# Performance work log

Measured on AMD Instinct MI355X. Metric: run time of the kernel, lower is better.

## Reference

```python
import jax, jax.numpy as jnp
import numpy as np

N, K, C, D4, HID, HEAD, DEPTH = 40000, 16, 128, 32, 512, 256, 4
EPS = 1e-5  # BatchNorm eps; eval mode with running_mean=0, running_var=1


def _bn(x, g, b):
    # eval-mode BatchNorm1d with fresh running stats (mean=0, var=1)
    return x * (g / np.sqrt(1.0 + EPS)) + b


def _mlp(x, w1, b1, w2, g, b):
    # Linear -> GELU -> Linear(no bias) -> BN
    return _bn(jax.nn.gelu(x @ w1 + b1) @ w2, g, b)


def _lfp(x, lxyz, knn, proj, coor, scale, g, b):
    # LFP: Linear(no bias) -> la_spse_a4 (neighbor gather + anisotropic spatial
    # positional encoding, one PE channel per 4 feature channels, max-pool over k) -> BN
    xp = x @ proj                                   # (N, C)
    xn = xp[knn]                                    # (N, K, C) irregular gather
    rel3 = (lxyz[knn] - lxyz[:, None])[..., :3]     # (N, K, 3)
    pe = jnp.einsum('nkc,cd->nkd', rel3, coor) * jnp.square(scale)  # (N, K, D4)
    out = jnp.max(xn.reshape(N, K, D4, 4) + pe[..., None], axis=1).reshape(N, C)
    return _bn(out, g, b)


def _knn_spse4(lxyz, feat, knn, m_sp, c, h):
    # knn_spse_4: squared anisotropic spatial distances (3 learned 4-d directions
    # per output channel, 12 params) + per-channel color (3) + height (1) weighted
    # squared diffs, averaged over k neighbors; caller takes sqrt.
    rel4 = lxyz[knn] - lxyz[:, None]                # (N, K, 4)
    relf = feat[knn] - feat[:, None]                # (N, K, 4) = color(3)+height(1)
    dirs = m_sp.reshape(3, 4, C)
    e = jnp.zeros((N, K, C), jnp.float32)
    for j in range(3):  # fixed small loop over 3 learned directions
        e = e + jnp.square(jnp.einsum('nkc,cd->nkd', rel4, dirs[j]))
    e = e + jnp.einsum('nki,id->nkd', jnp.square(relf[..., :3]), jnp.square(c))
    e = e + jnp.square(relf[..., 3:4]) * jnp.square(h)
    return jnp.sqrt(e.mean(axis=1))                 # (N, C)


def setup_inputs():
    key = jax.random.key(0)
    ks = jax.random.split(key, 32)
    rn = lambda i, s, sc=0.02: jax.random.normal(ks[i], s, jnp.float32) * sc
    gm = lambda i, s: 1.0 + jax.random.normal(ks[i], s, jnp.float32) * 0.1
    return {
        'x': rn(0, (N, 4), 1.0),
        'xyz': jax.random.uniform(ks[1], (N, 3), jnp.float32),
        'knn': jax.random.randint(ks[2], (N, K), 0, N, jnp.int32),
        'spse_m': rn(3, (12, C), 0.5),
        'spse_c': rn(4, (3, C), 0.5),
        'spse_h': rn(5, (C,), 0.5),
        'nbr_bn0_g': gm(6, (C,)), 'nbr_bn0_b': rn(7, (C,)),
        'nbr_w1': rn(8, (C, 2 * C)), 'nbr_b1': rn(9, (2 * C,)),
        'nbr_w2': rn(10, (2 * C, C)),
        'nbr_bn_g': gm(11, (C,)), 'nbr_bn_b': rn(12, (C,)),
        'lfp_proj': rn(13, (DEPTH, C, C)),
        'lfp_coor': rn(14, (DEPTH, 3, D4), 0.5),
        'lfp_scale': 0.1 + rn(15, (DEPTH, D4), 0.01),
        'lfp_bng': gm(16, (DEPTH, C)), 'lfp_bnb': rn(17, (DEPTH, C)),
        'mlp_w1': rn(18, (3, C, HID)), 'mlp_b1': rn(19, (3, HID)),
        'mlp_w2': rn(20, (3, HID, C)),
        'mlp_bng': gm(21, (3, C)), 'mlp_bnb': rn(22, (3, C)),
        'post_bn_g': gm(23, (C,)), 'post_bn_b': rn(24, (C,)),
        'post_w': rn(25, (C, HEAD)),
    }


def reference(x, xyz, knn, spse_m, spse_c, spse_h, nbr_bn0_g, nbr_bn0_b,
              nbr_w1, nbr_b1, nbr_w2, nbr_bn_g, nbr_bn_b,
              lfp_proj, lfp_coor, lfp_scale, lfp_bng, lfp_bnb,
              mlp_w1, mlp_b1, mlp_w2, mlp_bng, mlp_bnb,
              post_bn_g, post_bn_b, post_w):
    # Stage.forward, first==last stage, eval mode (no drop_path, no closs).
    lxyz = jnp.pad(xyz, ((0, 0), (0, 1)))  # cor_std = 1.0
    nbr = _knn_spse4(lxyz, x, knn, spse_m, spse_c, spse_h)
    nbr = _bn(nbr, nbr_bn0_g, nbr_bn0_b)
    nbr = jax.nn.gelu(nbr @ nbr_w1 + nbr_b1) @ nbr_w2   # nbr_proj
    h = _bn(nbr, nbr_bn_g, nbr_bn_b)                    # nbr_bn; x = nbr (first stage)
    # Block: residual MLP, then DEPTH LFPs with an MLP after every 2nd LFP
    h = h + _mlp(h, mlp_w1[0], mlp_b1[0], mlp_w2[0], mlp_bng[0], mlp_bnb[0])
    for i in range(DEPTH):
        h = h + _lfp(h, lxyz, knn, lfp_proj[i], lfp_coor[i], lfp_scale[i],
                     lfp_bng[i], lfp_bnb[i])
        if i % 2 == 1:
            j = i // 2 + 1
            h = h + _mlp(h, mlp_w1[j], mlp_b1[j], mlp_w2[j], mlp_bng[j], mlp_bnb[j])
    return _bn(h, post_bn_g, post_bn_b) @ post_w        # postproj -> (N, HEAD)
```

## Files before the change

kernel.cpp:

```cpp
#include <hip/hip_runtime.h>
#include <hip/hip_bf16.h>
#include <math.h>

#define NPTS 40000
#define KNB 16
#define CH 128

typedef unsigned short u16;
typedef __attribute__((ext_vector_type(8))) short bf16x8;
typedef __attribute__((ext_vector_type(4))) float f32x4;

__device__ __forceinline__ float gelu_f(float v) {
  const float u = 0.7978845608028654f * (v + 0.044715f * v * v * v);
  const float t = __builtin_amdgcn_exp2f(-2.8853900817779268f * u);
  return v * __builtin_amdgcn_rcpf(1.0f + t);
}

__device__ __forceinline__ float bnscale(float g) {
  return g * rsqrtf(1.0f + 1e-5f);
}

__device__ __forceinline__ u16 f2bf(float x) {
  union { __hip_bfloat16 b; u16 u; } cv;
  cv.b = __float2bfloat16(x);
  return cv.u;
}

__device__ __forceinline__ float bf2f(u16 u) {
  union { float f; unsigned int i; } cv;
  cv.i = ((unsigned int)u) << 16;
  return cv.f;
}

__device__ __forceinline__ void bf16split(float x, u16& hi, u16& lo) {
  hi = f2bf(x);
  lo = f2bf(x - bf2f(hi));
}

__device__ __forceinline__ void gl2lds(const u16* gp, u16* lp) {
  __builtin_amdgcn_global_load_lds(
      (const __attribute__((address_space(1))) void*)gp,
      (__attribute__((address_space(3))) void*)lp, 16, 0, 0);
}

__global__ __launch_bounds__(128) void spse_kernel(
    const float* __restrict__ x, const float* __restrict__ xyz,
    const int* __restrict__ knn, const float* __restrict__ sm,
    const float* __restrict__ sc, const float* __restrict__ sh,
    const float* __restrict__ g0, const float* __restrict__ b0,
    u16* __restrict__ oh, u16* __restrict__ ol) {
  const int n = blockIdx.x;
  const int c = threadIdx.x;
  __shared__ float sr[KNB][3];
  __shared__ float sf[KNB][4];
  if (c < KNB) {
    const int j = knn[n * KNB + c];
    sr[c][0] = xyz[j * 3 + 0] - xyz[n * 3 + 0];
    sr[c][1] = xyz[j * 3 + 1] - xyz[n * 3 + 1];
    sr[c][2] = xyz[j * 3 + 2] - xyz[n * 3 + 2];
    float f0 = x[j * 4 + 0] - x[n * 4 + 0];
    float f1 = x[j * 4 + 1] - x[n * 4 + 1];
    float f2 = x[j * 4 + 2] - x[n * 4 + 2];
    float f3 = x[j * 4 + 3] - x[n * 4 + 3];
    sf[c][0] = f0 * f0; sf[c][1] = f1 * f1;
    sf[c][2] = f2 * f2; sf[c][3] = f3 * f3;
  }
  __syncthreads();
  const float m0 = sm[c], m1 = sm[CH + c], m2 = sm[2 * CH + c];
  const float m4 = sm[4 * CH + c], m5 = sm[5 * CH + c], m6 = sm[6 * CH + c];
  const float m8 = sm[8 * CH + c], m9 = sm[9 * CH + c], m10 = sm[10 * CH + c];
  float c0 = sc[c];          c0 *= c0;
  float c1 = sc[CH + c];     c1 *= c1;
  float c2 = sc[2 * CH + c]; c2 *= c2;
  float h2 = sh[c];          h2 *= h2;
  float e = 0.0f;
#pragma unroll
  for (int k = 0; k < KNB; k++) {
    const float r0 = sr[k][0], r1 = sr[k][1], r2 = sr[k][2];
    const float d0 = fmaf(r2, m2, fmaf(r1, m1, r0 * m0));
    const float d1 = fmaf(r2, m6, fmaf(r1, m5, r0 * m4));
    const float d2 = fmaf(r2, m10, fmaf(r1, m9, r0 * m8));
    e = fmaf(d0, d0, e);
    e = fmaf(d1, d1, e);
    e = fmaf(d2, d2, e);
    e = fmaf(sf[k][0], c0, e);
    e = fmaf(sf[k][1], c1, e);
    e = fmaf(sf[k][2], c2, e);
    e = fmaf(sf[k][3], h2, e);
  }
  const float v = sqrtf(e * (1.0f / KNB)) * bnscale(g0[c]) + b0[c];
  u16 hi, lo; bf16split(v, hi, lo);
  const size_t idx = (size_t)n * CH + c;
  oh[idx] = hi; ol[idx] = lo;
}

template <bool XP>
__global__ __launch_bounds__(256, 4) void lfp_kernel(
    const u16* __restrict__ xp, const int* __restrict__ knn,
    const float* __restrict__ xyz, const float* __restrict__ coor,
    const float* __restrict__ scale, const float* __restrict__ g,
    const float* __restrict__ b, const u16* __restrict__ pjh,
    const u16* __restrict__ pjl, u16* __restrict__ xpo,
    u16* __restrict__ hh, u16* __restrict__ hl) {
  const int t = threadIdx.x;
  const int bid = blockIdx.x;
  __shared__ int si[16][KNB];
  __shared__ float sr[16][KNB][3];
  __shared__ __align__(16) u16 Hs[16 * 128];
  {
    const int pp = t >> 4, kk = t & 15;
    const int n = bid * 16 + pp;
    const int j = knn[n * KNB + kk];
    si[pp][kk] = j;
    sr[pp][kk][0] = xyz[j * 3 + 0] - xyz[n * 3 + 0];
    sr[pp][kk][1] = xyz[j * 3 + 1] - xyz[n * 3 + 1];
    sr[pp][kk][2] = xyz[j * 3 + 2] - xyz[n * 3 + 2];
  }
  __syncthreads();
  const int p = t >> 4, d8 = t & 15;
  const int n = bid * 16 + p;

  bf16x8 v[KNB];
#pragma unroll
  for (int k = 0; k < KNB; k++)
    v[k] = *(const bf16x8*)(xp + (size_t)si[p][k] * CH + d8 * 8);

  const float c0a = coor[d8 * 2],     c1a = coor[32 + d8 * 2],     c2a = coor[64 + d8 * 2];
  const float c0b = coor[d8 * 2 + 1], c1b = coor[32 + d8 * 2 + 1], c2b = coor[64 + d8 * 2 + 1];
  float s2a = scale[d8 * 2];     s2a *= s2a;
  float s2b = scale[d8 * 2 + 1]; s2b *= s2b;
  float a[8];
#pragma unroll
  for (int e = 0; e < 8; e++) a[e] = -3.0e38f;
#pragma unroll
  for (int k = 0; k < KNB; k++) {
    const float r0 = sr[p][k][0], r1 = sr[p][k][1], r2 = sr[p][k][2];
    const float pea = fmaf(r2, c2a, fmaf(r1, c1a, r0 * c0a)) * s2a;
    const float peb = fmaf(r2, c2b, fmaf(r1, c1b, r0 * c0b)) * s2b;
#pragma unroll
    for (int e = 0; e < 4; e++) a[e] = fmaxf(a[e], bf2f((u16)v[k][e]) + pea);
#pragma unroll
    for (int e = 4; e < 8; e++) a[e] = fmaxf(a[e], bf2f((u16)v[k][e]) + peb);
  }
  const size_t off = (size_t)n * CH + d8 * 8;
  union { u16 a[8]; uint4 v; } ih, il, oh, ol;
  ih.v = *(const uint4*)(hh + off);
  il.v = *(const uint4*)(hl + off);
#pragma unroll
  for (int e = 0; e < 8; e++) {
    const int c = d8 * 8 + e;
    const float nv = bf2f(ih.a[e]) + bf2f(il.a[e]) + a[e] * bnscale(g[c]) + b[c];
    u16 hi, lo; bf16split(nv, hi, lo);
    oh.a[e] = hi; ol.a[e] = lo;
  }
  *(uint4*)(hh + off) = oh.v;
  *(uint4*)(hl + off) = ol.v;

  if constexpr (XP) {
    {
      const int c0 = d8 * 8;
      const int cs0 = (c0 & ~63) | ((c0 & 63) ^ ((p & 7) << 3));
      *(uint4*)(Hs + p * 128 + cs0) = oh.v;
    }
    __syncthreads();
    const int lane = t & 63, w = t >> 6;
    const int lc = lane & 15, lq = lane >> 4;
    const int lq8 = lq * 8, lq4 = lq * 4;
    bf16x8 ph_[2][4], pl_[2][4];
#pragma unroll
    for (int nf = 0; nf < 2; nf++)
#pragma unroll
      for (int ks = 0; ks < 4; ks++) {
        const size_t wo = (size_t)(w * 32 + nf * 16 + lc) * 128 + ks * 32 + lq8;
        ph_[nf][ks] = *(const bf16x8*)(pjh + wo);
        pl_[nf][ks] = *(const bf16x8*)(pjl + wo);
      }
    const f32x4 zz = {0.0f, 0.0f, 0.0f, 0.0f};
    f32x4 xacc[2] = {zz, zz};
#pragma unroll
    for (int ks = 0; ks < 4; ks++) {
      const int j = ks * 32 + lq8;
      const int cs = (j & ~63) | ((j & 63) ^ ((lc & 7) << 3));
      const bf16x8 aF = *(const bf16x8*)(Hs + lc * 128 + cs);
#pragma unroll
      for (int nf = 0; nf < 2; nf++) {
        xacc[nf] = __builtin_amdgcn_mfma_f32_16x16x32_bf16(aF, ph_[nf][ks], xacc[nf], 0, 0, 0);
        xacc[nf] = __builtin_amdgcn_mfma_f32_16x16x32_bf16(aF, pl_[nf][ks], xacc[nf], 0, 0, 0);
      }
    }
#pragma unroll
    for (int q = 0; q < 4; q++)
#pragma unroll
      for (int nf = 0; nf < 2; nf++)
        xpo[(size_t)(bid * 16 + lq4 + q) * CH + w * 32 + nf * 16 + lc] =
            f2bf(xacc[nf][q]);
  }
}

__global__ __launch_bounds__(256) void prep_weights(
    const float* __restrict__ nw1, const float* __restrict__ nw2,
    const float* __restrict__ mw1, const float* __restrict__ mw2,
    const float* __restrict__ lproj, const float* __restrict__ pw,
    const float* __restrict__ pg, u16* __restrict__ th, u16* __restrict__ tl) {
  const int idx = blockIdx.x * 256 + threadIdx.x;
  const float* src;
  int local, Kd, Nd, dst, swz;
  float scale = 1.0f;
  if (idx < 32768)        { src = nw1; local = idx;          Kd = 128; Nd = 256; dst = 0; swz = 0; }
  else if (idx < 65536)   { src = nw2; local = idx - 32768;  Kd = 256; Nd = 128; dst = 32768; swz = 1; }
  else if (idx < 262144)  { int j = (idx - 65536) >> 16;  local = (idx - 65536) & 65535;
                            src = mw1 + j * 65536; Kd = 128; Nd = 512; dst = 65536 + j * 65536; swz = 0; }
  else if (idx < 458752)  { int j = (idx - 262144) >> 16; local = (idx - 262144) & 65535;
                            src = mw2 + j * 65536; Kd = 512; Nd = 128; dst = 262144 + j * 65536; swz = 1; }
  else if (idx < 524288)  { int i = (idx - 458752) >> 14; local = (idx - 458752) & 16383;
                            src = lproj + i * 16384; Kd = 128; Nd = 128; dst = 458752 + i * 16384; swz = 0; }
  else if (idx < 557056)  { local = idx - 524288; src = pw; Kd = 128; Nd = 256; dst = 524288; swz = 0;
                            scale = bnscale(pg[local >> 8]); }
  else return;
  const int k = local / Nd, n = local % Nd;
  const float v = src[local] * scale;
  u16 hi, lo; bf16split(v, hi, lo);
  const int ks = swz ? ((k & ~63) | ((k & 63) ^ ((n & 7) << 3))) : k;
  const int o = dst + n * Kd + ks;
  th[o] = hi; tl[o] = lo;
}

__global__ __launch_bounds__(256) void fold_pb(const float* __restrict__ pw,
                                               const float* __restrict__ pb,
                                               float* __restrict__ fb) {
  const int t = threadIdx.x;
  float a = 0.0f;
  for (int k = 0; k < 128; k++) a = fmaf(pb[k], pw[k * 256 + t], a);
  fb[t] = a;
}

template <int EPI, int NSPLIT>
__global__ __launch_bounds__(256, 2) void k128_reg(
    const u16* __restrict__ Ahi, const u16* __restrict__ Alo,
    const u16* __restrict__ Wth, const u16* __restrict__ Wtl,
    const float* __restrict__ p0, u16* __restrict__ outu,
    float* __restrict__ outf, int ostride, int ntiles) {
  const int t = threadIdx.x, lane = t & 63, w = t >> 6;
  const int col0 = blockIdx.y * 128;
  const int wm0 = (w >> 1) * 32, wn0 = (w & 1) * 64;
  const int lc = lane & 15, lq = lane >> 4;
  const int lq8 = lq * 8, lq4 = lq * 4;

  bf16x8 wh[4][4], wl[4][4];
  float bv[4];
#pragma unroll
  for (int nf = 0; nf < 4; nf++) {
    const int nr = col0 + wn0 + nf * 16 + lc;
    const u16* wr = Wth + (size_t)nr * 128;
    const u16* wr2 = Wtl + (size_t)nr * 128;
#pragma unroll
    for (int ks = 0; ks < 4; ks++) {
      wh[nf][ks] = *(const bf16x8*)(wr + ks * 32 + lq8);
      wl[nf][ks] = *(const bf16x8*)(wr2 + ks * 32 + lq8);
    }
    bv[nf] = p0[nr];
  }

  const f32x4 zz = {0.0f, 0.0f, 0.0f, 0.0f};
  for (int tile = blockIdx.x; tile < ntiles; tile += gridDim.x) {
    const int row0 = tile * 64;
    f32x4 acc[2][4];
#pragma unroll
    for (int mf = 0; mf < 2; mf++)
#pragma unroll
      for (int nf = 0; nf < 4; nf++) acc[mf][nf] = zz;
#pragma unroll
    for (int ks = 0; ks < 4; ks++) {
      bf16x8 ah[2], al[2];
#pragma unroll
      for (int mf = 0; mf < 2; mf++) {
        const size_t ao = (size_t)(row0 + wm0 + mf * 16 + lc) * 128 + ks * 32 + lq8;
        ah[mf] = *(const bf16x8*)(Ahi + ao);
        if (NSPLIT == 3) al[mf] = *(const bf16x8*)(Alo + ao);
      }
#pragma unroll
      for (int mf = 0; mf < 2; mf++)
#pragma unroll
        for (int nf = 0; nf < 4; nf++) {
          acc[mf][nf] = __builtin_amdgcn_mfma_f32_16x16x32_bf16(ah[mf], wh[nf][ks], acc[mf][nf], 0, 0, 0);
          acc[mf][nf] = __builtin_amdgcn_mfma_f32_16x16x32_bf16(ah[mf], wl[nf][ks], acc[mf][nf], 0, 0, 0);
          if (NSPLIT == 3)
            acc[mf][nf] = __builtin_amdgcn_mfma_f32_16x16x32_bf16(al[mf], wh[nf][ks], acc[mf][nf], 0, 0, 0);
        }
    }
#pragma unroll
    for (int mf = 0; mf < 2; mf++)
#pragma unroll
      for (int q = 0; q < 4; q++) {
        const int r = row0 + wm0 + mf * 16 + lq4 + q;
#pragma unroll
        for (int nf = 0; nf < 4; nf++) {
          const int col = col0 + wn0 + nf * 16 + lc;
          const size_t off = (size_t)r * ostride + col;
          const float v = acc[mf][nf][q];
          if (EPI == 1) outu[off] = f2bf(gelu_f(v + bv[nf]));
          else          outf[off] = v + bv[nf];
        }
      }
  }
}

template <int K, bool RES, bool XP>
__global__ __launch_bounds__(256, 3) void gemm_w2(
    const u16* __restrict__ A, const u16* __restrict__ Wth,
    const u16* __restrict__ Wtl, const float* __restrict__ g,
    const float* __restrict__ bb, const u16* __restrict__ pjh,
    const u16* __restrict__ pjl, u16* __restrict__ xpo,
    u16* __restrict__ hh, u16* __restrict__ hl) {
  __shared__ __align__(16) u16 Ws[2][128 * 64];
  const int t = threadIdx.x, lane = t & 63, w = t >> 6;
  const int row0 = blockIdx.x * 64;
  const int wm0 = (w >> 1) * 32, wn0 = (w & 1) * 64;
  const int lc = lane & 15, lq = lane >> 4;
  const int lq8 = lq * 8, lq4 = lq * 4;

  const f32x4 zz = {0.0f, 0.0f, 0.0f, 0.0f};
  f32x4 acc[2][4];
#pragma unroll
  for (int mf = 0; mf < 2; mf++)
#pragma unroll
    for (int nf = 0; nf < 4; nf++) acc[mf][nf] = zz;

  auto stage_slab = [&](u16* lds, int kb) {
#pragma unroll
    for (int i = 0; i < 1024; i += 256) {
      const int wc0 = i + w * 64;
      const int c = wc0 + lane;
      gl2lds(Wth + (size_t)(c >> 3) * K + kb + (c & 7) * 8, lds + wc0 * 8);
    }
  };
  auto load_af = [&](bf16x8 (&dst)[2][2], int kb) {
#pragma unroll
    for (int mf = 0; mf < 2; mf++)
#pragma unroll
      for (int ks = 0; ks < 2; ks++)
        dst[mf][ks] = *(const bf16x8*)(A + (size_t)(row0 + wm0 + mf * 16 + lc) * K +
                                       kb + ks * 32 + lq8);
  };

  bf16x8 afc[2][2], afn[2][2];
  stage_slab(Ws[0], 0);
  load_af(afc, 0);
  __syncthreads();

  constexpr int NT = K / 64;
#pragma unroll 2
  for (int tt = 0; tt < NT; tt++) {
    const int cur = tt & 1;
    if (tt + 1 < NT) {
      stage_slab(Ws[cur ^ 1], (tt + 1) * 64);
      load_af(afn, (tt + 1) * 64);
    }
#pragma unroll
    for (int ks = 0; ks < 2; ks++) {
      bf16x8 whf[4], wlf[4];
#pragma unroll
      for (int nf = 0; nf < 4; nf++) {
        const int nr = wn0 + nf * 16 + lc;
        const int j = (ks * 32 + lq8) ^ ((nr & 7) << 3);
        whf[nf] = *(const bf16x8*)(Ws[cur] + nr * 64 + j);
        wlf[nf] = *(const bf16x8*)(Wtl + (size_t)nr * K + tt * 64 + j);
      }
#pragma unroll
      for (int mf = 0; mf < 2; mf++)
#pragma unroll
        for (int nf = 0; nf < 4; nf++) {
          acc[mf][nf] = __builtin_amdgcn_mfma_f32_16x16x32_bf16(afc[mf][ks], whf[nf], acc[mf][nf], 0, 0, 0);
          acc[mf][nf] = __builtin_amdgcn_mfma_f32_16x16x32_bf16(afc[mf][ks], wlf[nf], acc[mf][nf], 0, 0, 0);
        }
    }
    __syncthreads();
#pragma unroll
    for (int mf = 0; mf < 2; mf++)
#pragma unroll
      for (int ks = 0; ks < 2; ks++) afc[mf][ks] = afn[mf][ks];
  }

  u16* Hs = &Ws[0][0];
  float S0[4], S1[4];
#pragma unroll
  for (int nf = 0; nf < 4; nf++) {
    const int col = wn0 + nf * 16 + lc;
    S0[nf] = bnscale(g[col]);
    S1[nf] = bb[col];
  }
#pragma unroll
  for (int mf = 0; mf < 2; mf++)
#pragma unroll
    for (int q = 0; q < 4; q++) {
      const int r = row0 + wm0 + mf * 16 + lq4 + q;
#pragma unroll
      for (int nf = 0; nf < 4; nf++) {
        const int col = wn0 + nf * 16 + lc;
        const size_t off = (size_t)r * CH + col;
        float v = acc[mf][nf][q] * S0[nf] + S1[nf];
        if (RES) v += bf2f(hh[off]) + bf2f(hl[off]);
        u16 hi, lo; bf16split(v, hi, lo);
        hh[off] = hi; hl[off] = lo;
        if constexpr (XP) {
          const int rl = wm0 + mf * 16 + lq4 + q;
          const int cs = (col & ~63) | ((col & 63) ^ ((rl & 7) << 3));
          Hs[rl * 128 + cs] = hi;
        }
      }
    }

  if constexpr (XP) {
    __syncthreads();
    bf16x8 ph_[2][4], pl_[2][4];
#pragma unroll
    for (int nf = 0; nf < 2; nf++)
#pragma unroll
      for (int ks = 0; ks < 4; ks++) {
        const size_t wo = (size_t)(w * 32 + nf * 16 + lc) * 128 + ks * 32 + lq8;
        ph_[nf][ks] = *(const bf16x8*)(pjh + wo);
        pl_[nf][ks] = *(const bf16x8*)(pjl + wo);
      }
    f32x4 xacc[4][2];
#pragma unroll
    for (int mf = 0; mf < 4; mf++)
#pragma unroll
      for (int nf = 0; nf < 2; nf++) xacc[mf][nf] = zz;
#pragma unroll
    for (int ks = 0; ks < 4; ks++) {
      const int j = ks * 32 + lq8;
      bf16x8 aF[4];
#pragma unroll
      for (int mf = 0; mf < 4; mf++) {
        const int r = mf * 16 + lc;
        const int cs = (j & ~63) | ((j & 63) ^ ((r & 7) << 3));
        aF[mf] = *(const bf16x8*)(Hs + r * 128 + cs);
      }
#pragma unroll
      for (int mf = 0; mf < 4; mf++)
#pragma unroll
        for (int nf = 0; nf < 2; nf++) {
          xacc[mf][nf] = __builtin_amdgcn_mfma_f32_16x16x32_bf16(aF[mf], ph_[nf][ks], xacc[mf][nf], 0, 0, 0);
          xacc[mf][nf] = __builtin_amdgcn_mfma_f32_16x16x32_bf16(aF[mf], pl_[nf][ks], xacc[mf][nf], 0, 0, 0);
        }
    }
#pragma unroll
    for (int mf = 0; mf < 4; mf++)
#pragma unroll
      for (int q = 0; q < 4; q++)
#pragma unroll
        for (int nf = 0; nf < 2; nf++)
          xpo[(size_t)(row0 + mf * 16 + lq4 + q) * CH + w * 32 + nf * 16 + lc] =
              f2bf(xacc[mf][nf][q]);
  }
}

extern "C" void kernel_launch(void* const* d_in, const int* in_sizes, int n_in,
                              void* d_out, int out_size, void* d_ws, size_t ws_size,
                              hipStream_t stream) {
  const float* x    = (const float*)d_in[0];
  const float* xyz  = (const float*)d_in[1];
  const int*   knn  = (const int*)d_in[2];
  const float* sm   = (const float*)d_in[3];
  const float* scc  = (const float*)d_in[4];
  const float* shh  = (const float*)d_in[5];
  const float* bn0g = (const float*)d_in[6];
  const float* bn0b = (const float*)d_in[7];
  const float* nw1  = (const float*)d_in[8];
  const float* nb1  = (const float*)d_in[9];
  const float* nw2  = (const float*)d_in[10];
  const float* nbng = (const float*)d_in[11];
  const float* nbnb = (const float*)d_in[12];
  const float* lproj  = (const float*)d_in[13];
  const float* lcoor  = (const float*)d_in[14];
  const float* lscale = (const float*)d_in[15];
  const float* lbng   = (const float*)d_in[16];
  const float* lbnb   = (const float*)d_in[17];
  const float* mw1  = (const float*)d_in[18];
  const float* mb1  = (const float*)d_in[19];
  const float* mw2  = (const float*)d_in[20];
  const float* mbng = (const float*)d_in[21];
  const float* mbnb = (const float*)d_in[22];
  const float* pg   = (const float*)d_in[23];
  const float* pb   = (const float*)d_in[24];
  const float* pw   = (const float*)d_in[25];
  float* out = (float*)d_out;

  char* ws = (char*)d_ws;
  u16*   h_hi = (u16*)(ws + 0);
  u16*   h_lo = (u16*)(ws + 10240000);
  u16*   act  = (u16*)(ws + 20480000);
  u16*   xpA  = (u16*)(ws + 61440000);
  u16*   xpB  = (u16*)(ws + 71680000);
  u16*   Wh   = (u16*)(ws + 81920000);
  u16*   Wl   = (u16*)(ws + 83034112);
  float* fb   = (float*)(ws + 84148224);

  const u16* nw1t   = Wh + 0;
  const u16* nw2t   = Wh + 32768;
  const u16* mw1t   = Wh + 65536;
  const u16* mw2t   = Wh + 262144;
  const u16* lprojt = Wh + 458752;
  const u16* postt  = Wh + 524288;
  const u16* nw1tl   = Wl + 0;
  const u16* nw2tl   = Wl + 32768;
  const u16* mw1tl   = Wl + 65536;
  const u16* mw2tl   = Wl + 262144;
  const u16* lprojtl = Wl + 458752;
  const u16* posttl  = Wl + 524288;

  prep_weights<<<2176, 256, 0, stream>>>(nw1, nw2, mw1, mw2, lproj, pw, pg, Wh, Wl);
  fold_pb<<<1, 256, 0, stream>>>(pw, pb, fb);

  spse_kernel<<<NPTS, 128, 0, stream>>>(x, xyz, knn, sm, scc, shh, bn0g, bn0b, h_hi, h_lo);

  k128_reg<1, 2><<<dim3(256, 2), 256, 0, stream>>>(h_hi, h_lo, nw1t, nw1tl, nb1,
                                                   act, nullptr, 256, 625);
  gemm_w2<256, false, false><<<625, 256, 0, stream>>>(
      act, nw2t, nw2tl, nbng, nbnb, nullptr, nullptr, nullptr, h_hi, h_lo);

  k128_reg<1, 2><<<dim3(128, 4), 256, 0, stream>>>(h_hi, h_lo, mw1t, mw1tl, mb1,
                                                   act, nullptr, 512, 625);
  gemm_w2<512, true, true><<<625, 256, 0, stream>>>(
      act, mw2t, mw2tl, mbng, mbnb, lprojt, lprojtl, xpA, h_hi, h_lo);

  lfp_kernel<true><<<2500, 256, 0, stream>>>(
      xpA, knn, xyz, lcoor + 0 * 96, lscale + 0 * 32, lbng + 0 * 128, lbnb + 0 * 128,
      lprojt + 16384, lprojtl + 16384, xpB, h_hi, h_lo);

  lfp_kernel<false><<<2500, 256, 0, stream>>>(
      xpB, knn, xyz, lcoor + 1 * 96, lscale + 1 * 32, lbng + 1 * 128, lbnb + 1 * 128,
      nullptr, nullptr, nullptr, h_hi, h_lo);
  k128_reg<1, 2><<<dim3(128, 4), 256, 0, stream>>>(h_hi, h_lo, mw1t + 65536,
                                                   mw1tl + 65536, mb1 + 512,
                                                   act, nullptr, 512, 625);
  gemm_w2<512, true, true><<<625, 256, 0, stream>>>(
      act, mw2t + 65536, mw2tl + 65536, mbng + 128, mbnb + 128,
      lprojt + 2 * 16384, lprojtl + 2 * 16384, xpA, h_hi, h_lo);

  lfp_kernel<true><<<2500, 256, 0, stream>>>(
      xpA, knn, xyz, lcoor + 2 * 96, lscale + 2 * 32, lbng + 2 * 128, lbnb + 2 * 128,
      lprojt + 3 * 16384, lprojtl + 3 * 16384, xpB, h_hi, h_lo);

  lfp_kernel<false><<<2500, 256, 0, stream>>>(
      xpB, knn, xyz, lcoor + 3 * 96, lscale + 3 * 32, lbng + 3 * 128, lbnb + 3 * 128,
      nullptr, nullptr, nullptr, h_hi, h_lo);
  k128_reg<1, 2><<<dim3(128, 4), 256, 0, stream>>>(h_hi, h_lo, mw1t + 2 * 65536,
                                                   mw1tl + 2 * 65536, mb1 + 2 * 512,
                                                   act, nullptr, 512, 625);
  gemm_w2<512, true, false><<<625, 256, 0, stream>>>(
      act, mw2t + 2 * 65536, mw2tl + 2 * 65536, mbng + 2 * 128, mbnb + 2 * 128,
      nullptr, nullptr, nullptr, h_hi, h_lo);

  k128_reg<2, 3><<<dim3(256, 2), 256, 0, stream>>>(h_hi, h_lo, postt, posttl, fb,
                                                   nullptr, out, 256, 625);
}
```

Before: 428.4 us.

## Store LFP projections channel-blocked and split LFP gather by channel quarter

The xp projection buffer changes from point-major [N][128] to four channel-quarter blocks [4][N][32], so each LFP block gathers neighbours from a 2.56 MB slice that fits in cache better. The LFP kernel now handles 64 points times one 32-channel quarter per block. It also issues the residual loads early behind a sched_barrier. The projection previously fused into the LFP kernel moves into a separate k128_reg GEMM launch with a new EPI==0 path that writes the blocked layout. This adds two kernel launches and an extra round trip of h through memory, in exchange for better gather locality.

```diff
diff --git a/kernel.cpp b/kernel.cpp
--- a/kernel.cpp
+++ b/kernel.cpp
@@ -94,22 +94,20 @@
   oh[idx] = hi; ol[idx] = lo;
 }
 
-template <bool XP>
 __global__ __launch_bounds__(256, 4) void lfp_kernel(
     const u16* __restrict__ xp, const int* __restrict__ knn,
     const float* __restrict__ xyz, const float* __restrict__ coor,
     const float* __restrict__ scale, const float* __restrict__ g,
-    const float* __restrict__ b, const u16* __restrict__ pjh,
-    const u16* __restrict__ pjl, u16* __restrict__ xpo,
-    u16* __restrict__ hh, u16* __restrict__ hl) {
+    const float* __restrict__ b, u16* __restrict__ hh, u16* __restrict__ hl) {
   const int t = threadIdx.x;
   const int bid = blockIdx.x;
-  __shared__ int si[16][KNB];
-  __shared__ float sr[16][KNB][3];
-  __shared__ __align__(16) u16 Hs[16 * 128];
-  {
-    const int pp = t >> 4, kk = t & 15;
-    const int n = bid * 16 + pp;
+  const int q = bid & 3;
+  const int pg = bid >> 2;
+  __shared__ int si[64][KNB];
+  __shared__ float sr[64][KNB][3];
+  for (int i = t; i < 64 * KNB; i += 256) {
+    const int pp = i >> 4, kk = i & 15;
+    const int n = pg * 64 + pp;
     const int j = knn[n * KNB + kk];
     si[pp][kk] = j;
     sr[pp][kk][0] = xyz[j * 3 + 0] - xyz[n * 3 + 0];
@@ -117,18 +115,27 @@
     sr[pp][kk][2] = xyz[j * 3 + 2] - xyz[n * 3 + 2];
   }
   __syncthreads();
-  const int p = t >> 4, d8 = t & 15;
-  const int n = bid * 16 + p;
-
+  const int p = t >> 2;
+  const int l = t & 3;
+  const int n = pg * 64 + p;
+  const int cbase = q * 32 + l * 8;
+  const int d0 = cbase >> 2;
+
+  const u16* xpq = xp + (size_t)q * NPTS * 32;
   bf16x8 v[KNB];
 #pragma unroll
   for (int k = 0; k < KNB; k++)
-    v[k] = *(const bf16x8*)(xp + (size_t)si[p][k] * CH + d8 * 8);
-
-  const float c0a = coor[d8 * 2],     c1a = coor[32 + d8 * 2],     c2a = coor[64 + d8 * 2];
-  const float c0b = coor[d8 * 2 + 1], c1b = coor[32 + d8 * 2 + 1], c2b = coor[64 + d8 * 2 + 1];
-  float s2a = scale[d8 * 2];     s2a *= s2a;
-  float s2b = scale[d8 * 2 + 1]; s2b *= s2b;
+    v[k] = *(const bf16x8*)(xpq + (size_t)si[p][k] * 32 + l * 8);
+  const size_t off = (size_t)n * CH + cbase;
+  union { u16 a[8]; uint4 v; } ih, il, oh, ol;
+  ih.v = *(const uint4*)(hh + off);
+  il.v = *(const uint4*)(hl + off);
+  __builtin_amdgcn_sched_barrier(0);
+
+  const float c0a = coor[d0],     c1a = coor[32 + d0],     c2a = coor[64 + d0];
+  const float c0b = coor[d0 + 1], c1b = coor[32 + d0 + 1], c2b = coor[64 + d0 + 1];
+  float s2a = scale[d0];     s2a *= s2a;
+  float s2b = scale[d0 + 1]; s2b *= s2b;
   float a[8];
 #pragma unroll
   for (int e = 0; e < 8; e++) a[e] = -3.0e38f;
@@ -142,59 +149,15 @@
 #pragma unroll
     for (int e = 4; e < 8; e++) a[e] = fmaxf(a[e], bf2f((u16)v[k][e]) + peb);
   }
-  const size_t off = (size_t)n * CH + d8 * 8;
-  union { u16 a[8]; uint4 v; } ih, il, oh, ol;
-  ih.v = *(const uint4*)(hh + off);
-  il.v = *(const uint4*)(hl + off);
 #pragma unroll
   for (int e = 0; e < 8; e++) {
-    const int c = d8 * 8 + e;
+    const int c = cbase + e;
     const float nv = bf2f(ih.a[e]) + bf2f(il.a[e]) + a[e] * bnscale(g[c]) + b[c];
     u16 hi, lo; bf16split(nv, hi, lo);
     oh.a[e] = hi; ol.a[e] = lo;
   }
   *(uint4*)(hh + off) = oh.v;
   *(uint4*)(hl + off) = ol.v;
-
-  if constexpr (XP) {
-    {
-      const int c0 = d8 * 8;
-      const int cs0 = (c0 & ~63) | ((c0 & 63) ^ ((p & 7) << 3));
-      *(uint4*)(Hs + p * 128 + cs0) = oh.v;
-    }
-    __syncthreads();
-    const int lane = t & 63, w = t >> 6;
-    const int lc = lane & 15, lq = lane >> 4;
-    const int lq8 = lq * 8, lq4 = lq * 4;
-    bf16x8 ph_[2][4], pl_[2][4];
-#pragma unroll
-    for (int nf = 0; nf < 2; nf++)
-#pragma unroll
-      for (int ks = 0; ks < 4; ks++) {
-        const size_t wo = (size_t)(w * 32 + nf * 16 + lc) * 128 + ks * 32 + lq8;
-        ph_[nf][ks] = *(const bf16x8*)(pjh + wo);
-        pl_[nf][ks] = *(const bf16x8*)(pjl + wo);
-      }
-    const f32x4 zz = {0.0f, 0.0f, 0.0f, 0.0f};
-    f32x4 xacc[2] = {zz, zz};
-#pragma unroll
-    for (int ks = 0; ks < 4; ks++) {
-      const int j = ks * 32 + lq8;
-      const int cs = (j & ~63) | ((j & 63) ^ ((lc & 7) << 3));
-      const bf16x8 aF = *(const bf16x8*)(Hs + lc * 128 + cs);
-#pragma unroll
-      for (int nf = 0; nf < 2; nf++) {
-        xacc[nf] = __builtin_amdgcn_mfma_f32_16x16x32_bf16(aF, ph_[nf][ks], xacc[nf], 0, 0, 0);
-        xacc[nf] = __builtin_amdgcn_mfma_f32_16x16x32_bf16(aF, pl_[nf][ks], xacc[nf], 0, 0, 0);
-      }
-    }
-#pragma unroll
-    for (int q = 0; q < 4; q++)
-#pragma unroll
-      for (int nf = 0; nf < 2; nf++)
-        xpo[(size_t)(bid * 16 + lq4 + q) * CH + w * 32 + nf * 16 + lc] =
-            f2bf(xacc[nf][q]);
-  }
 }
 
 __global__ __launch_bounds__(256) void prep_weights(
@@ -258,7 +221,7 @@
       wh[nf][ks] = *(const bf16x8*)(wr + ks * 32 + lq8);
       wl[nf][ks] = *(const bf16x8*)(wr2 + ks * 32 + lq8);
     }
-    bv[nf] = p0[nr];
+    bv[nf] = (EPI == 0) ? 0.0f : p0[nr];
   }
 
   const f32x4 zz = {0.0f, 0.0f, 0.0f, 0.0f};
@@ -296,10 +259,13 @@
 #pragma unroll
         for (int nf = 0; nf < 4; nf++) {
           const int col = col0 + wn0 + nf * 16 + lc;
-          const size_t off = (size_t)r * ostride + col;
           const float v = acc[mf][nf][q];
-          if (EPI == 1) outu[off] = f2bf(gelu_f(v + bv[nf]));
-          else          outf[off] = v + bv[nf];
+          if (EPI == 0)
+            outu[((size_t)(col >> 5) * NPTS + r) * 32 + (col & 31)] = f2bf(v);
+          else if (EPI == 1)
+            outu[(size_t)r * ostride + col] = f2bf(gelu_f(v + bv[nf]));
+          else
+            outf[(size_t)r * ostride + col] = v + bv[nf];
         }
       }
   }
@@ -450,7 +416,7 @@
       for (int q = 0; q < 4; q++)
 #pragma unroll
         for (int nf = 0; nf < 2; nf++)
-          xpo[(size_t)(row0 + mf * 16 + lq4 + q) * CH + w * 32 + nf * 16 + lc] =
+          xpo[((size_t)w * NPTS + (row0 + mf * 16 + lq4 + q)) * 32 + nf * 16 + lc] =
               f2bf(xacc[mf][nf][q]);
   }
 }
@@ -524,13 +490,16 @@
   gemm_w2<512, true, true><<<625, 256, 0, stream>>>(
       act, mw2t, mw2tl, mbng, mbnb, lprojt, lprojtl, xpA, h_hi, h_lo);
 
-  lfp_kernel<true><<<2500, 256, 0, stream>>>(
+  lfp_kernel<<<2500, 256, 0, stream>>>(
       xpA, knn, xyz, lcoor + 0 * 96, lscale + 0 * 32, lbng + 0 * 128, lbnb + 0 * 128,
-      lprojt + 16384, lprojtl + 16384, xpB, h_hi, h_lo);
-
-  lfp_kernel<false><<<2500, 256, 0, stream>>>(
+      h_hi, h_lo);
+  k128_reg<0, 2><<<dim3(625, 1), 256, 0, stream>>>(h_hi, h_lo, lprojt + 16384,
+                                                   lprojtl + 16384, nullptr,
+                                                   xpB, nullptr, 128, 625);
+
+  lfp_kernel<<<2500, 256, 0, stream>>>(
       xpB, knn, xyz, lcoor + 1 * 96, lscale + 1 * 32, lbng + 1 * 128, lbnb + 1 * 128,
-      nullptr, nullptr, nullptr, h_hi, h_lo);
+      h_hi, h_lo);
   k128_reg<1, 2><<<dim3(128, 4), 256, 0, stream>>>(h_hi, h_lo, mw1t + 65536,
                                                    mw1tl + 65536, mb1 + 512,
                                                    act, nullptr, 512, 625);
@@ -538,13 +507,16 @@
       act, mw2t + 65536, mw2tl + 65536, mbng + 128, mbnb + 128,
       lprojt + 2 * 16384, lprojtl + 2 * 16384, xpA, h_hi, h_lo);
 
-  lfp_kernel<true><<<2500, 256, 0, stream>>>(
+  lfp_kernel<<<2500, 256, 0, stream>>>(
       xpA, knn, xyz, lcoor + 2 * 96, lscale + 2 * 32, lbng + 2 * 128, lbnb + 2 * 128,
-      lprojt + 3 * 16384, lprojtl + 3 * 16384, xpB, h_hi, h_lo);
-
-  lfp_kernel<false><<<2500, 256, 0, stream>>>(
+      h_hi, h_lo);
+  k128_reg<0, 2><<<dim3(625, 1), 256, 0, stream>>>(h_hi, h_lo, lprojt + 3 * 16384,
+                                                   lprojtl + 3 * 16384, nullptr,
+                                                   xpB, nullptr, 128, 625);
+
+  lfp_kernel<<<2500, 256, 0, stream>>>(
       xpB, knn, xyz, lcoor + 3 * 96, lscale + 3 * 32, lbng + 3 * 128, lbnb + 3 * 128,
-      nullptr, nullptr, nullptr, h_hi, h_lo);
+      h_hi, h_lo);
   k128_reg<1, 2><<<dim3(128, 4), 256, 0, stream>>>(h_hi, h_lo, mw1t + 2 * 65536,
                                                    mw1tl + 2 * 65536, mb1 + 2 * 512,
                                                    act, nullptr, 512, 625);
```

Result: slower. 464.5 us (+8.4%).

## Split LFP neighbor max across thread pairs with 4-point blocks

Applied to the files above, without the earlier changes.

Each LFP block now handles 4 points with 128 threads instead of 16 points with 256 threads. Each pair of threads splits the 16 neighbors and combines partial maxima through shared memory. The aim is more independent gathers in flight and higher occupancy by halving per-thread register use. The fused projection MFMA now computes 16 rows of which only 4 are valid, wasting three quarters of the MFMA work. It also reloads projection weights from global memory in every one of the 10000 blocks.

```diff
diff --git a/kernel.cpp b/kernel.cpp
--- a/kernel.cpp
+++ b/kernel.cpp
@@ -95,7 +95,7 @@
 }
 
 template <bool XP>
-__global__ __launch_bounds__(256, 4) void lfp_kernel(
+__global__ __launch_bounds__(128, 4) void lfp_kernel(
     const u16* __restrict__ xp, const int* __restrict__ knn,
     const float* __restrict__ xyz, const float* __restrict__ coor,
     const float* __restrict__ scale, const float* __restrict__ g,
@@ -104,12 +104,13 @@
     u16* __restrict__ hh, u16* __restrict__ hl) {
   const int t = threadIdx.x;
   const int bid = blockIdx.x;
-  __shared__ int si[16][KNB];
-  __shared__ float sr[16][KNB][3];
-  __shared__ __align__(16) u16 Hs[16 * 128];
-  {
+  __shared__ int si[4][KNB];
+  __shared__ float sr[4][KNB][3];
+  __shared__ float pmax[4][16][8];
+  __shared__ __align__(16) u16 Hs[4 * 128];
+  if (t < 64) {
     const int pp = t >> 4, kk = t & 15;
-    const int n = bid * 16 + pp;
+    const int n = bid * 4 + pp;
     const int j = knn[n * KNB + kk];
     si[pp][kk] = j;
     sr[pp][kk][0] = xyz[j * 3 + 0] - xyz[n * 3 + 0];
@@ -117,13 +118,15 @@
     sr[pp][kk][2] = xyz[j * 3 + 2] - xyz[n * 3 + 2];
   }
   __syncthreads();
-  const int p = t >> 4, d8 = t & 15;
-  const int n = bid * 16 + p;
-
-  bf16x8 v[KNB];
-#pragma unroll
-  for (int k = 0; k < KNB; k++)
-    v[k] = *(const bf16x8*)(xp + (size_t)si[p][k] * CH + d8 * 8);
+  const int p = t >> 5;
+  const int d8 = (t >> 1) & 15;
+  const int kh = t & 1;
+  const int n = bid * 4 + p;
+
+  bf16x8 v[8];
+#pragma unroll
+  for (int k = 0; k < 8; k++)
+    v[k] = *(const bf16x8*)(xp + (size_t)si[p][kh * 8 + k] * CH + d8 * 8);
 
   const float c0a = coor[d8 * 2],     c1a = coor[32 + d8 * 2],     c2a = coor[64 + d8 * 2];
   const float c0b = coor[d8 * 2 + 1], c1b = coor[32 + d8 * 2 + 1], c2b = coor[64 + d8 * 2 + 1];
@@ -133,8 +136,9 @@
 #pragma unroll
   for (int e = 0; e < 8; e++) a[e] = -3.0e38f;
 #pragma unroll
-  for (int k = 0; k < KNB; k++) {
-    const float r0 = sr[p][k][0], r1 = sr[p][k][1], r2 = sr[p][k][2];
+  for (int k = 0; k < 8; k++) {
+    const int kk = kh * 8 + k;
+    const float r0 = sr[p][kk][0], r1 = sr[p][kk][1], r2 = sr[p][kk][2];
     const float pea = fmaf(r2, c2a, fmaf(r1, c1a, r0 * c0a)) * s2a;
     const float peb = fmaf(r2, c2b, fmaf(r1, c1b, r0 * c0b)) * s2b;
 #pragma unroll
@@ -142,58 +146,62 @@
 #pragma unroll
     for (int e = 4; e < 8; e++) a[e] = fmaxf(a[e], bf2f((u16)v[k][e]) + peb);
   }
-  const size_t off = (size_t)n * CH + d8 * 8;
-  union { u16 a[8]; uint4 v; } ih, il, oh, ol;
-  ih.v = *(const uint4*)(hh + off);
-  il.v = *(const uint4*)(hl + off);
-#pragma unroll
-  for (int e = 0; e < 8; e++) {
-    const int c = d8 * 8 + e;
-    const float nv = bf2f(ih.a[e]) + bf2f(il.a[e]) + a[e] * bnscale(g[c]) + b[c];
-    u16 hi, lo; bf16split(nv, hi, lo);
-    oh.a[e] = hi; ol.a[e] = lo;
-  }
-  *(uint4*)(hh + off) = oh.v;
-  *(uint4*)(hl + off) = ol.v;
-
-  if constexpr (XP) {
-    {
+  if (kh == 1) {
+#pragma unroll
+    for (int e = 0; e < 8; e++) pmax[p][d8][e] = a[e];
+  }
+  __syncthreads();
+  if (kh == 0) {
+    const size_t off = (size_t)n * CH + d8 * 8;
+    union { u16 a[8]; uint4 v; } ih, il, oh, ol;
+    ih.v = *(const uint4*)(hh + off);
+    il.v = *(const uint4*)(hl + off);
+#pragma unroll
+    for (int e = 0; e < 8; e++) {
+      const float am = fmaxf(a[e], pmax[p][d8][e]);
+      const int c = d8 * 8 + e;
+      const float nv = bf2f(ih.a[e]) + bf2f(il.a[e]) + am * bnscale(g[c]) + b[c];
+      u16 hi, lo; bf16split(nv, hi, lo);
+      oh.a[e] = hi; ol.a[e] = lo;
+    }
+    *(uint4*)(hh + off) = oh.v;
+    *(uint4*)(hl + off) = ol.v;
+    if constexpr (XP) {
       const int c0 = d8 * 8;
       const int cs0 = (c0 & ~63) | ((c0 & 63) ^ ((p & 7) << 3));
       *(uint4*)(Hs + p * 128 + cs0) = oh.v;
     }
+  }
+
+  if constexpr (XP) {
     __syncthreads();
     const int lane = t & 63, w = t >> 6;
     const int lc = lane & 15, lq = lane >> 4;
     const int lq8 = lq * 8, lq4 = lq * 4;
-    bf16x8 ph_[2][4], pl_[2][4];
-#pragma unroll
-    for (int nf = 0; nf < 2; nf++)
-#pragma unroll
-      for (int ks = 0; ks < 4; ks++) {
-        const size_t wo = (size_t)(w * 32 + nf * 16 + lc) * 128 + ks * 32 + lq8;
-        ph_[nf][ks] = *(const bf16x8*)(pjh + wo);
-        pl_[nf][ks] = *(const bf16x8*)(pjl + wo);
-      }
     const f32x4 zz = {0.0f, 0.0f, 0.0f, 0.0f};
-    f32x4 xacc[2] = {zz, zz};
+    f32x4 xacc[4] = {zz, zz, zz, zz};
 #pragma unroll
     for (int ks = 0; ks < 4; ks++) {
       const int j = ks * 32 + lq8;
       const int cs = (j & ~63) | ((j & 63) ^ ((lc & 7) << 3));
       const bf16x8 aF = *(const bf16x8*)(Hs + lc * 128 + cs);
 #pragma unroll
-      for (int nf = 0; nf < 2; nf++) {
-        xacc[nf] = __builtin_amdgcn_mfma_f32_16x16x32_bf16(aF, ph_[nf][ks], xacc[nf], 0, 0, 0);
-        xacc[nf] = __builtin_amdgcn_mfma_f32_16x16x32_bf16(aF, pl_[nf][ks], xacc[nf], 0, 0, 0);
-      }
-    }
-#pragma unroll
-    for (int q = 0; q < 4; q++)
-#pragma unroll
-      for (int nf = 0; nf < 2; nf++)
-        xpo[(size_t)(bid * 16 + lq4 + q) * CH + w * 32 + nf * 16 + lc] =
-            f2bf(xacc[nf][q]);
+      for (int nf = 0; nf < 4; nf++) {
+        const size_t wo = (size_t)(w * 64 + nf * 16 + lc) * 128 + ks * 32 + lq8;
+        const bf16x8 ph = *(const bf16x8*)(pjh + wo);
+        const bf16x8 pl = *(const bf16x8*)(pjl + wo);
+        xacc[nf] = __builtin_amdgcn_mfma_f32_16x16x32_bf16(aF, ph, xacc[nf], 0, 0, 0);
+        xacc[nf] = __builtin_amdgcn_mfma_f32_16x16x32_bf16(aF, pl, xacc[nf], 0, 0, 0);
+      }
+    }
+    if (lq == 0) {
+#pragma unroll
+      for (int q = 0; q < 4; q++)
+#pragma unroll
+        for (int nf = 0; nf < 4; nf++)
+          xpo[(size_t)(bid * 4 + q) * CH + w * 64 + nf * 16 + lc] =
+              f2bf(xacc[nf][q]);
+    }
   }
 }
 
@@ -524,11 +532,11 @@
   gemm_w2<512, true, true><<<625, 256, 0, stream>>>(
       act, mw2t, mw2tl, mbng, mbnb, lprojt, lprojtl, xpA, h_hi, h_lo);
 
-  lfp_kernel<true><<<2500, 256, 0, stream>>>(
+  lfp_kernel<true><<<10000, 128, 0, stream>>>(
       xpA, knn, xyz, lcoor + 0 * 96, lscale + 0 * 32, lbng + 0 * 128, lbnb + 0 * 128,
       lprojt + 16384, lprojtl + 16384, xpB, h_hi, h_lo);
 
-  lfp_kernel<false><<<2500, 256, 0, stream>>>(
+  lfp_kernel<false><<<10000, 128, 0, stream>>>(
       xpB, knn, xyz, lcoor + 1 * 96, lscale + 1 * 32, lbng + 1 * 128, lbnb + 1 * 128,
       nullptr, nullptr, nullptr, h_hi, h_lo);
   k128_reg<1, 2><<<dim3(128, 4), 256, 0, stream>>>(h_hi, h_lo, mw1t + 65536,
@@ -538,11 +546,11 @@
       act, mw2t + 65536, mw2tl + 65536, mbng + 128, mbnb + 128,
       lprojt + 2 * 16384, lprojtl + 2 * 16384, xpA, h_hi, h_lo);
 
-  lfp_kernel<true><<<2500, 256, 0, stream>>>(
+  lfp_kernel<true><<<10000, 128, 0, stream>>>(
       xpA, knn, xyz, lcoor + 2 * 96, lscale + 2 * 32, lbng + 2 * 128, lbnb + 2 * 128,
       lprojt + 3 * 16384, lprojtl + 3 * 16384, xpB, h_hi, h_lo);
 
-  lfp_kernel<false><<<2500, 256, 0, stream>>>(
+  lfp_kernel<false><<<10000, 128, 0, stream>>>(
       xpB, knn, xyz, lcoor + 3 * 96, lscale + 3 * 32, lbng + 3 * 128, lbnb + 3 * 128,
       nullptr, nullptr, nullptr, h_hi, h_lo);
   k128_reg<1, 2><<<dim3(128, 4), 256, 0, stream>>>(h_hi, h_lo, mw1t + 2 * 65536,
```

Result: slower. 527.7 us (+23.2%).
